# Kernel optimization log

Measured on AMD Instinct MI355X. Metric: run time of the kernel, lower is better.

## Reference

```python
import jax, jax.numpy as jnp
import numpy as np

N_NODES = 100000
N_EDGES = 1600000
IN_CH = 128
HID = 128   # 2 * out_channels
OUT_CH = 64


def setup_inputs() -> dict:
    key = jax.random.key(0)
    k1, k2, k3, k4, k5, k6 = jax.random.split(key, 6)
    x = jax.random.normal(k1, (N_NODES, IN_CH), dtype=jnp.float32)
    edge_index = jax.random.randint(k2, (2, N_EDGES), 0, N_NODES, dtype=jnp.int64)
    W1 = jax.random.normal(k3, (IN_CH, HID), dtype=jnp.float32) / np.sqrt(IN_CH)
    b1 = jax.random.normal(k4, (HID,), dtype=jnp.float32) * 0.01
    W2 = jax.random.normal(k5, (HID, OUT_CH), dtype=jnp.float32) / np.sqrt(HID)
    b2 = jax.random.normal(k6, (OUT_CH,), dtype=jnp.float32) * 0.01
    return {"x": x, "edge_index": edge_index, "W1": W1, "b1": b1, "W2": W2, "b2": b2}


def _gcn_layer(x, src, dst, norm, W, b, n_nodes):
    # GCNConv: linear transform, then normalized scatter-add aggregation + bias
    h = x @ W                                   # [N, d_out]
    msg = h[src] * norm[:, None]                # gather + edge normalize, [E+N, d_out]
    out = jax.ops.segment_sum(msg, dst, num_segments=n_nodes)
    return out + b


def reference(x, edge_index, W1, b1, W2, b2):
    n = x.shape[0]
    loop = jnp.arange(n, dtype=edge_index.dtype)
    # add self-loops (PyG GCNConv default)
    src = jnp.concatenate([edge_index[0], loop])
    dst = jnp.concatenate([edge_index[1], loop])
    # symmetric normalization deg^-1/2[src] * deg^-1/2[dst]
    deg = jax.ops.segment_sum(jnp.ones_like(dst, x.dtype), dst, num_segments=n)
    dinv = jnp.where(deg > 0, jax.lax.rsqrt(deg), 0.0)
    norm = dinv[src] * dinv[dst]

    h = jax.nn.relu(_gcn_layer(x, src, dst, norm, W1, b1, n))
    out = jax.nn.relu(_gcn_layer(h, src, dst, norm, W2, b2, n))
    return out
```

## Files before the change

### kernel.cpp

```cpp
#include <hip/hip_runtime.h>
#include <hip/hip_fp16.h>

typedef _Float16 f16x8 __attribute__((ext_vector_type(8)));
typedef _Float16 f16x4 __attribute__((ext_vector_type(4)));
typedef float f32x4 __attribute__((ext_vector_type(4)));

#define BSH 9
#define BSZ 512
#define CAP 12288

__global__ __launch_bounds__(256) void passA(const int* __restrict__ ei,
                                             int* __restrict__ bcount, int E, int NB) {
  __shared__ int hist[256];
  int t = threadIdx.x;
  hist[t] = 0;
  __syncthreads();
  for (int e = blockIdx.x * 256 + t; e < E; e += gridDim.x * 256)
    atomicAdd(&hist[ei[E + e] >> BSH], 1);
  __syncthreads();
  if (t < NB && hist[t]) atomicAdd(&bcount[t], hist[t]);
}

__global__ __launch_bounds__(256) void scanB(const int* __restrict__ bcount,
                                             int* __restrict__ bstart,
                                             int* __restrict__ bfill, int NB, int E) {
  __shared__ int s[256];
  int t = threadIdx.x;
  int v = (t < NB) ? bcount[t] : 0;
  s[t] = v;
  __syncthreads();
  for (int off = 1; off < 256; off <<= 1) {
    int add = (t >= off) ? s[t - off] : 0;
    __syncthreads();
    s[t] += add;
    __syncthreads();
  }
  if (t < NB) {
    int ex = s[t] - v;
    bstart[t] = ex;
    bfill[t] = ex;
  }
  if (t == 0) bstart[NB] = E;
}

template <int NC, int NWC, bool IN_F16, bool SCALE>
__device__ __forceinline__ void gemm_mfma_body(
    const void* __restrict__ Xv, const float* __restrict__ W,
    const float* __restrict__ dinv, _Float16* __restrict__ G, int nrows, int bid,
    _Float16* Bs) {
  int t = threadIdx.x;
  {
    int n = t % NC;
    int kh = (t / NC) * (NC / 2);
    constexpr int NBLK = (NC / 2) / 8;
#pragma unroll
    for (int b = 0; b < NBLK; ++b) {
      f16x8 tmp;
#pragma unroll
      for (int j = 0; j < 8; ++j)
        tmp[j] = (_Float16)W[(size_t)(kh + b * 8 + j) * NC + n];
      *(f16x8*)(&Bs[n * 136 + kh + b * 8]) = tmp;
    }
  }
  __syncthreads();

  int w = t >> 6, lane = t & 63;
  int m = lane & 15, q = lane >> 4;
  int wr = (w / NWC) * 64, wc = (w % NWC) * 64;
  int row0 = bid * ((4 / NWC) * 64);

  f32x4 acc[4][4];
#pragma unroll
  for (int rt = 0; rt < 4; ++rt)
#pragma unroll
    for (int ct = 0; ct < 4; ++ct)
#pragma unroll
      for (int qq = 0; qq < 4; ++qq) acc[rt][ct][qq] = 0.f;

#pragma unroll
  for (int kc = 0; kc < 4; ++kc) {
    int kbase = kc * 32 + q * 8;
    f16x8 af[4];
#pragma unroll
    for (int rt = 0; rt < 4; ++rt) {
      int row = row0 + wr + rt * 16 + m;
      if constexpr (IN_F16) {
        f16x8 a = {0, 0, 0, 0, 0, 0, 0, 0};
        if (row < nrows) a = *(const f16x8*)((const _Float16*)Xv + (size_t)row * 128 + kbase);
        af[rt] = a;
      } else {
        float4 x0 = {0, 0, 0, 0}, x1 = {0, 0, 0, 0};
        if (row < nrows) {
          const float* Xf = (const float*)Xv;
          x0 = *(const float4*)(Xf + (size_t)row * 128 + kbase);
          x1 = *(const float4*)(Xf + (size_t)row * 128 + kbase + 4);
        }
        f16x8 a;
        a[0] = (_Float16)x0.x; a[1] = (_Float16)x0.y;
        a[2] = (_Float16)x0.z; a[3] = (_Float16)x0.w;
        a[4] = (_Float16)x1.x; a[5] = (_Float16)x1.y;
        a[6] = (_Float16)x1.z; a[7] = (_Float16)x1.w;
        af[rt] = a;
      }
    }
    f16x8 bf[4];
#pragma unroll
    for (int ct = 0; ct < 4; ++ct) {
      int n = wc + ct * 16 + m;
      bf[ct] = *(f16x8*)(&Bs[n * 136 + kbase]);
    }
#pragma unroll
    for (int rt = 0; rt < 4; ++rt)
#pragma unroll
      for (int ct = 0; ct < 4; ++ct)
        acc[rt][ct] = __builtin_amdgcn_mfma_f32_16x16x32_f16(af[rt], bf[ct],
                                                             acc[rt][ct], 0, 0, 0);
  }
#pragma unroll
  for (int rt = 0; rt < 4; ++rt) {
#pragma unroll
    for (int r = 0; r < 4; ++r) {
      int row = row0 + wr + rt * 16 + q * 4 + r;
      if (row < nrows) {
        float d = SCALE ? dinv[row] : 1.f;
#pragma unroll
        for (int ct = 0; ct < 4; ++ct) {
          int col = wc + ct * 16 + m;
          G[(size_t)row * NC + col] = (_Float16)(acc[rt][ct][r] * d);
        }
      }
    }
  }
}

__global__ __launch_bounds__(256) void fused_gemm_passB(
    const float* __restrict__ X, const float* __restrict__ W1,
    _Float16* __restrict__ G, int nrows, int GB,
    const int* __restrict__ ei, int* __restrict__ bfill,
    unsigned int* __restrict__ pairs, int E, int PB) {
  __shared__ char smem[128 * 136 * 2];
  int g = blockIdx.x;
  int M2 = 2 * (GB < PB ? GB : PB);
  bool is_gemm;
  int bid;
  if (g < M2) { is_gemm = (g & 1) == 0; bid = g >> 1; }
  else        { is_gemm = (GB > PB);    bid = g - M2 + (GB < PB ? GB : PB); }
  if (is_gemm) {
    gemm_mfma_body<128, 2, false, false>(X, W1, nullptr, G, nrows, bid,
                                         (_Float16*)smem);
  } else {
    int* hist = (int*)smem;
    int* gbase = (int*)(smem + 1024);
    int t = threadIdx.x;
    hist[t] = 0;
    __syncthreads();
    int d[8], s[8], lp[8], bb[8];
    int base = bid * 2048;
#pragma unroll
    for (int u = 0; u < 8; ++u) {
      int e = base + u * 256 + t;
      if (e < E) {
        d[u] = ei[E + e];
        s[u] = ei[e];
        bb[u] = d[u] >> BSH;
        lp[u] = atomicAdd(&hist[bb[u]], 1);
      } else {
        bb[u] = -1;
      }
    }
    __syncthreads();
    if (hist[t]) gbase[t] = atomicAdd(&bfill[t], hist[t]);
    __syncthreads();
#pragma unroll
    for (int u = 0; u < 8; ++u)
      if (bb[u] >= 0)
        pairs[gbase[bb[u]] + lp[u]] =
            ((unsigned int)(d[u] & (BSZ - 1)) << 17) | (unsigned int)s[u];
  }
}

__global__ __launch_bounds__(256) void gemm2_mfma(const _Float16* __restrict__ X,
                                                  const float* __restrict__ W,
                                                  const float* __restrict__ dinv,
                                                  _Float16* __restrict__ G, int nrows) {
  __shared__ _Float16 Bs[64 * 136];
  gemm_mfma_body<64, 1, true, true>(X, W, dinv, G, nrows, blockIdx.x, Bs);
}

__global__ __launch_bounds__(512) void passC(const unsigned int* __restrict__ pairs,
                                             const int* __restrict__ bstart,
                                             int* __restrict__ rowstart,
                                             int* __restrict__ deg,
                                             float* __restrict__ dinv,
                                             int* __restrict__ csr, int N) {
  __shared__ int hcnt[BSZ];
  __shared__ int lfill[BSZ];
  __shared__ int ss[512];
  __shared__ int lcsr[CAP];
  int b = blockIdx.x;
  int t = threadIdx.x;
  int lo = bstart[b], hi = bstart[b + 1];
  int cnt = hi - lo;
  int nbase = b << BSH;
  hcnt[t] = 0;
  __syncthreads();
  for (int k = lo + t; k < hi; k += 512)
    atomicAdd(&hcnt[(pairs[k] >> 17) & (BSZ - 1)], 1);
  __syncthreads();
  int v = hcnt[t];
  ss[t] = v;
  __syncthreads();
  for (int off = 1; off < 512; off <<= 1) {
    int add = (t >= off) ? ss[t - off] : 0;
    __syncthreads();
    ss[t] += add;
    __syncthreads();
  }
  int ex = ss[t] - v;
  lfill[t] = ex;
  int node = nbase + t;
  if (node < N) {
    rowstart[node] = lo + ex;
    deg[node] = v;
    dinv[node] = rsqrtf((float)(v + 1));
  }
  __syncthreads();
  bool fits = (cnt <= CAP);
  for (int k = lo + t; k < hi; k += 512) {
    unsigned int p = pairs[k];
    int pos = atomicAdd(&lfill[(p >> 17) & (BSZ - 1)], 1);
    int src = (int)(p & 0x1FFFFu);
    if (fits) lcsr[pos] = src;
    else      csr[lo + pos] = src;
  }
  __syncthreads();
  if (fits)
    for (int k = t; k < cnt; k += 512) csr[lo + k] = lcsr[k];
}

__global__ __launch_bounds__(256) void agg128(
    const __half* __restrict__ G, const int* __restrict__ csr,
    const int* __restrict__ rowstart, const int* __restrict__ deg,
    const float* __restrict__ dinv, const float* __restrict__ bias,
    __half* __restrict__ out, int n) {
  int wid = blockIdx.x * 4 + (threadIdx.x >> 6);
  if (wid >= n) return;
  int i = __builtin_amdgcn_readfirstlane(wid);
  int lane = threadIdx.x & 63;
  int g = lane >> 4;
  int c = lane & 15;
  const _Float16* Gh = (const _Float16*)G;
  float di = dinv[i];
  f16x8 self = *(const f16x8*)(Gh + (size_t)i * 128 + c * 8);
  float wself = (g == 0) ? di : 0.f;
  float a[8];
#pragma unroll
  for (int j = 0; j < 8; ++j) a[j] = wself * (float)self[j];
  int s = rowstart[i];
  int d = deg[i];
  for (int base = 0; base < d; base += 64) {
    int chunk = d - base;
    if (chunk > 64) chunk = 64;
    int myidx = (lane < chunk) ? csr[s + base + lane] : i;
    for (int k = 0; k < chunk; k += 8) {
      int sl0 = k + g, sl1 = k + 4 + g;
      int s0 = __shfl(myidx, sl0);
      int s1 = __shfl(myidx, sl1);
      float w0 = dinv[s0];
      float w1 = dinv[s1];
      if (sl0 >= chunk) w0 = 0.f;
      if (sl1 >= chunk) w1 = 0.f;
      f16x8 v0 = *(const f16x8*)(Gh + (size_t)s0 * 128 + c * 8);
      f16x8 v1 = *(const f16x8*)(Gh + (size_t)s1 * 128 + c * 8);
#pragma unroll
      for (int j = 0; j < 8; ++j) a[j] = fmaf(w0, (float)v0[j], a[j]);
#pragma unroll
      for (int j = 0; j < 8; ++j) a[j] = fmaf(w1, (float)v1[j], a[j]);
    }
  }
#pragma unroll
  for (int j = 0; j < 8; ++j) {
    a[j] += __shfl_xor(a[j], 16);
    a[j] += __shfl_xor(a[j], 32);
  }
  if (g == 0) {
    float4 b0 = *(const float4*)(bias + c * 8);
    float4 b1 = *(const float4*)(bias + c * 8 + 4);
    f16x8 r;
    r[0] = (_Float16)fmaxf(fmaf(di, a[0], b0.x), 0.f);
    r[1] = (_Float16)fmaxf(fmaf(di, a[1], b0.y), 0.f);
    r[2] = (_Float16)fmaxf(fmaf(di, a[2], b0.z), 0.f);
    r[3] = (_Float16)fmaxf(fmaf(di, a[3], b0.w), 0.f);
    r[4] = (_Float16)fmaxf(fmaf(di, a[4], b1.x), 0.f);
    r[5] = (_Float16)fmaxf(fmaf(di, a[5], b1.y), 0.f);
    r[6] = (_Float16)fmaxf(fmaf(di, a[6], b1.z), 0.f);
    r[7] = (_Float16)fmaxf(fmaf(di, a[7], b1.w), 0.f);
    *(f16x8*)((_Float16*)out + (size_t)i * 128 + c * 8) = r;
  }
}

__global__ __launch_bounds__(256) void agg64(
    const __half* __restrict__ G, const int* __restrict__ csr,
    const int* __restrict__ rowstart, const int* __restrict__ deg,
    const float* __restrict__ dinv, const float* __restrict__ bias,
    float* __restrict__ out, int n) {
  int wid = blockIdx.x * 4 + (threadIdx.x >> 6);
  if (wid >= n) return;
  int i = __builtin_amdgcn_readfirstlane(wid);
  int lane = threadIdx.x & 63;
  int g = lane >> 4;
  int c = lane & 15;
  const _Float16* Gh = (const _Float16*)G;
  f16x4 self = *(const f16x4*)(Gh + (size_t)i * 64 + c * 4);
  float wself = (g == 0) ? 1.f : 0.f;
  float a[4];
#pragma unroll
  for (int j = 0; j < 4; ++j) a[j] = wself * (float)self[j];
  int s = rowstart[i];
  int d = deg[i];
  for (int base = 0; base < d; base += 64) {
    int chunk = d - base;
    if (chunk > 64) chunk = 64;
    int myidx = (lane < chunk) ? csr[s + base + lane] : i;
    for (int k = 0; k < chunk; k += 8) {
      int sl0 = k + g, sl1 = k + 4 + g;
      int s0 = __shfl(myidx, sl0);
      int s1 = __shfl(myidx, sl1);
      float w0 = (sl0 < chunk) ? 1.f : 0.f;
      float w1 = (sl1 < chunk) ? 1.f : 0.f;
      f16x4 v0 = *(const f16x4*)(Gh + (size_t)s0 * 64 + c * 4);
      f16x4 v1 = *(const f16x4*)(Gh + (size_t)s1 * 64 + c * 4);
#pragma unroll
      for (int j = 0; j < 4; ++j) a[j] = fmaf(w0, (float)v0[j], a[j]);
#pragma unroll
      for (int j = 0; j < 4; ++j) a[j] = fmaf(w1, (float)v1[j], a[j]);
    }
  }
#pragma unroll
  for (int j = 0; j < 4; ++j) {
    a[j] += __shfl_xor(a[j], 16);
    a[j] += __shfl_xor(a[j], 32);
  }
  if (g == 0) {
    float di = dinv[i];
    float4 bv = *(const float4*)(bias + c * 4);
    float4 r;
    r.x = fmaxf(fmaf(di, a[0], bv.x), 0.f);
    r.y = fmaxf(fmaf(di, a[1], bv.y), 0.f);
    r.z = fmaxf(fmaf(di, a[2], bv.z), 0.f);
    r.w = fmaxf(fmaf(di, a[3], bv.w), 0.f);
    *(float4*)(out + (size_t)i * 64 + c * 4) = r;
  }
}

extern "C" void kernel_launch(void* const* d_in, const int* in_sizes, int n_in,
                              void* d_out, int out_size, void* d_ws, size_t ws_size,
                              hipStream_t stream) {
  const float* x  = (const float*)d_in[0];
  const int*   ei = (const int*)d_in[1];
  const float* W1 = (const float*)d_in[2];
  const float* b1 = (const float*)d_in[3];
  const float* W2 = (const float*)d_in[4];
  const float* b2 = (const float*)d_in[5];
  float* out = (float*)d_out;

  const int N = in_sizes[0] / 128;
  const int E = in_sizes[1] / 2;
  const int NB = (N + BSZ - 1) >> BSH;

  char* base = (char*)d_ws;
  size_t off = 0;
  auto alloc = [&](size_t bytes) -> void* {
    void* p = base + off;
    off += (bytes + 255) & ~(size_t)255;
    return p;
  };
  int*          bcount   = (int*)alloc(256 * 4);
  int*          bstart   = (int*)alloc(260 * 4);
  int*          bfill    = (int*)alloc(256 * 4);
  int*          deg      = (int*)alloc((size_t)N * 4);
  int*          rowstart = (int*)alloc((size_t)N * 4);
  float*        dinv     = (float*)alloc((size_t)N * 4);
  int*          csr      = (int*)alloc((size_t)E * 4);
  unsigned int* pairs    = (unsigned int*)alloc((size_t)E * 4);
  __half*       g1       = (__half*)alloc((size_t)N * 128 * 2);
  __half*       x2       = (__half*)alloc((size_t)N * 128 * 2);

  hipMemsetAsync(bcount, 0, 256 * 4, stream);
  passA<<<512, 256, 0, stream>>>(ei, bcount, E, NB);
  scanB<<<1, 256, 0, stream>>>(bcount, bstart, bfill, NB, E);

  int GB = (N + 127) / 128;
  int PB = (E + 2047) / 2048;
  fused_gemm_passB<<<GB + PB, 256, 0, stream>>>(x, W1, (_Float16*)g1, N, GB, ei,
                                                bfill, pairs, E, PB);
  passC<<<NB, 512, 0, stream>>>(pairs, bstart, rowstart, deg, dinv, csr, N);

  agg128<<<(N + 3) / 4, 256, 0, stream>>>(g1, csr, rowstart, deg, dinv, b1, x2, N);
  int G2B = (N + 255) / 256;
  gemm2_mfma<<<G2B, 256, 0, stream>>>((const _Float16*)x2, W2, dinv,
                                      (_Float16*)g1, N);
  agg64<<<(N + 3) / 4, 256, 0, stream>>>(g1, csr, rowstart, deg, dinv, b2, out, N);
}
```

Measured before the change: 282.4 us.

## Compute degrees early and fold source normalization into layer-1 GEMM

Degree counting moves into passA using global atomics, so the layer-1 GEMM can pre-scale rows by deg^-1/2. This lets agg128 drop its per-neighbor dinv gather and do plain sums. The dinv array is removed, and each kernel recomputes rsqrt from deg. Both aggregation kernels gain a 16-neighbor unrolled inner loop to raise memory-level parallelism. The cost is 1.6M global atomics in passA plus an extra memset.

```diff
diff --git a/kernel.cpp b/kernel.cpp
--- a/kernel.cpp
+++ b/kernel.cpp
@@ -1,5 +1,6 @@
 #include <hip/hip_runtime.h>
 #include <hip/hip_fp16.h>
+#include <math.h>
 
 typedef _Float16 f16x8 __attribute__((ext_vector_type(8)));
 typedef _Float16 f16x4 __attribute__((ext_vector_type(4)));
@@ -10,13 +11,17 @@
 #define CAP 12288
 
 __global__ __launch_bounds__(256) void passA(const int* __restrict__ ei,
-                                             int* __restrict__ bcount, int E, int NB) {
+                                             int* __restrict__ bcount,
+                                             int* __restrict__ deg, int E, int NB) {
   __shared__ int hist[256];
   int t = threadIdx.x;
   hist[t] = 0;
   __syncthreads();
-  for (int e = blockIdx.x * 256 + t; e < E; e += gridDim.x * 256)
-    atomicAdd(&hist[ei[E + e] >> BSH], 1);
+  for (int e = blockIdx.x * 256 + t; e < E; e += gridDim.x * 256) {
+    int d = ei[E + e];
+    atomicAdd(&hist[d >> BSH], 1);
+    atomicAdd(&deg[d], 1);
+  }
   __syncthreads();
   if (t < NB && hist[t]) atomicAdd(&bcount[t], hist[t]);
 }
@@ -46,7 +51,7 @@
 template <int NC, int NWC, bool IN_F16, bool SCALE>
 __device__ __forceinline__ void gemm_mfma_body(
     const void* __restrict__ Xv, const float* __restrict__ W,
-    const float* __restrict__ dinv, _Float16* __restrict__ G, int nrows, int bid,
+    const int* __restrict__ deg, _Float16* __restrict__ G, int nrows, int bid,
     _Float16* Bs) {
   int t = threadIdx.x;
   {
@@ -122,7 +127,7 @@
     for (int r = 0; r < 4; ++r) {
       int row = row0 + wr + rt * 16 + q * 4 + r;
       if (row < nrows) {
-        float d = SCALE ? dinv[row] : 1.f;
+        float d = SCALE ? rsqrtf((float)deg[row] + 1.f) : 1.f;
 #pragma unroll
         for (int ct = 0; ct < 4; ++ct) {
           int col = wc + ct * 16 + m;
@@ -135,7 +140,7 @@
 
 __global__ __launch_bounds__(256) void fused_gemm_passB(
     const float* __restrict__ X, const float* __restrict__ W1,
-    _Float16* __restrict__ G, int nrows, int GB,
+    const int* __restrict__ deg, _Float16* __restrict__ G, int nrows, int GB,
     const int* __restrict__ ei, int* __restrict__ bfill,
     unsigned int* __restrict__ pairs, int E, int PB) {
   __shared__ char smem[128 * 136 * 2];
@@ -146,8 +151,8 @@
   if (g < M2) { is_gemm = (g & 1) == 0; bid = g >> 1; }
   else        { is_gemm = (GB > PB);    bid = g - M2 + (GB < PB ? GB : PB); }
   if (is_gemm) {
-    gemm_mfma_body<128, 2, false, false>(X, W1, nullptr, G, nrows, bid,
-                                         (_Float16*)smem);
+    gemm_mfma_body<128, 2, false, true>(X, W1, deg, G, nrows, bid,
+                                        (_Float16*)smem);
   } else {
     int* hist = (int*)smem;
     int* gbase = (int*)(smem + 1024);
@@ -181,17 +186,15 @@
 
 __global__ __launch_bounds__(256) void gemm2_mfma(const _Float16* __restrict__ X,
                                                   const float* __restrict__ W,
-                                                  const float* __restrict__ dinv,
+                                                  const int* __restrict__ deg,
                                                   _Float16* __restrict__ G, int nrows) {
   __shared__ _Float16 Bs[64 * 136];
-  gemm_mfma_body<64, 1, true, true>(X, W, dinv, G, nrows, blockIdx.x, Bs);
+  gemm_mfma_body<64, 1, true, true>(X, W, deg, G, nrows, blockIdx.x, Bs);
 }
 
 __global__ __launch_bounds__(512) void passC(const unsigned int* __restrict__ pairs,
                                              const int* __restrict__ bstart,
                                              int* __restrict__ rowstart,
-                                             int* __restrict__ deg,
-                                             float* __restrict__ dinv,
                                              int* __restrict__ csr, int N) {
   __shared__ int hcnt[BSZ];
   __shared__ int lfill[BSZ];
@@ -219,11 +222,7 @@
   int ex = ss[t] - v;
   lfill[t] = ex;
   int node = nbase + t;
-  if (node < N) {
-    rowstart[node] = lo + ex;
-    deg[node] = v;
-    dinv[node] = rsqrtf((float)(v + 1));
-  }
+  if (node < N) rowstart[node] = lo + ex;
   __syncthreads();
   bool fits = (cnt <= CAP);
   for (int k = lo + t; k < hi; k += 512) {
@@ -241,8 +240,7 @@
 __global__ __launch_bounds__(256) void agg128(
     const __half* __restrict__ G, const int* __restrict__ csr,
     const int* __restrict__ rowstart, const int* __restrict__ deg,
-    const float* __restrict__ dinv, const float* __restrict__ bias,
-    __half* __restrict__ out, int n) {
+    const float* __restrict__ bias, __half* __restrict__ out, int n) {
   int wid = blockIdx.x * 4 + (threadIdx.x >> 6);
   if (wid >= n) return;
   int i = __builtin_amdgcn_readfirstlane(wid);
@@ -250,26 +248,43 @@
   int g = lane >> 4;
   int c = lane & 15;
   const _Float16* Gh = (const _Float16*)G;
-  float di = dinv[i];
+  int d = deg[i];
+  int s = rowstart[i];
+  float di = rsqrtf((float)d + 1.f);
   f16x8 self = *(const f16x8*)(Gh + (size_t)i * 128 + c * 8);
-  float wself = (g == 0) ? di : 0.f;
+  float wself = (g == 0) ? 1.f : 0.f;
   float a[8];
 #pragma unroll
   for (int j = 0; j < 8; ++j) a[j] = wself * (float)self[j];
-  int s = rowstart[i];
-  int d = deg[i];
   for (int base = 0; base < d; base += 64) {
     int chunk = d - base;
     if (chunk > 64) chunk = 64;
     int myidx = (lane < chunk) ? csr[s + base + lane] : i;
-    for (int k = 0; k < chunk; k += 8) {
+    int k = 0;
+    for (; k + 15 < chunk; k += 16) {
+      int s0 = __shfl(myidx, k + g);
+      int s1 = __shfl(myidx, k + 4 + g);
+      int s2 = __shfl(myidx, k + 8 + g);
+      int s3 = __shfl(myidx, k + 12 + g);
+      f16x8 v0 = *(const f16x8*)(Gh + (size_t)s0 * 128 + c * 8);
+      f16x8 v1 = *(const f16x8*)(Gh + (size_t)s1 * 128 + c * 8);
+      f16x8 v2 = *(const f16x8*)(Gh + (size_t)s2 * 128 + c * 8);
+      f16x8 v3 = *(const f16x8*)(Gh + (size_t)s3 * 128 + c * 8);
+#pragma unroll
+      for (int j = 0; j < 8; ++j) a[j] += (float)v0[j];
+#pragma unroll
+      for (int j = 0; j < 8; ++j) a[j] += (float)v1[j];
+#pragma unroll
+      for (int j = 0; j < 8; ++j) a[j] += (float)v2[j];
+#pragma unroll
+      for (int j = 0; j < 8; ++j) a[j] += (float)v3[j];
+    }
+    for (; k < chunk; k += 8) {
       int sl0 = k + g, sl1 = k + 4 + g;
       int s0 = __shfl(myidx, sl0);
       int s1 = __shfl(myidx, sl1);
-      float w0 = dinv[s0];
-      float w1 = dinv[s1];
-      if (sl0 >= chunk) w0 = 0.f;
-      if (sl1 >= chunk) w1 = 0.f;
+      float w0 = (sl0 < chunk) ? 1.f : 0.f;
+      float w1 = (sl1 < chunk) ? 1.f : 0.f;
       f16x8 v0 = *(const f16x8*)(Gh + (size_t)s0 * 128 + c * 8);
       f16x8 v1 = *(const f16x8*)(Gh + (size_t)s1 * 128 + c * 8);
 #pragma unroll
@@ -302,8 +317,7 @@
 __global__ __launch_bounds__(256) void agg64(
     const __half* __restrict__ G, const int* __restrict__ csr,
     const int* __restrict__ rowstart, const int* __restrict__ deg,
-    const float* __restrict__ dinv, const float* __restrict__ bias,
-    float* __restrict__ out, int n) {
+    const float* __restrict__ bias, float* __restrict__ out, int n) {
   int wid = blockIdx.x * 4 + (threadIdx.x >> 6);
   if (wid >= n) return;
   int i = __builtin_amdgcn_readfirstlane(wid);
@@ -311,18 +325,38 @@
   int g = lane >> 4;
   int c = lane & 15;
   const _Float16* Gh = (const _Float16*)G;
+  int d = deg[i];
+  int s = rowstart[i];
+  float di = rsqrtf((float)d + 1.f);
   f16x4 self = *(const f16x4*)(Gh + (size_t)i * 64 + c * 4);
   float wself = (g == 0) ? 1.f : 0.f;
   float a[4];
 #pragma unroll
   for (int j = 0; j < 4; ++j) a[j] = wself * (float)self[j];
-  int s = rowstart[i];
-  int d = deg[i];
   for (int base = 0; base < d; base += 64) {
     int chunk = d - base;
     if (chunk > 64) chunk = 64;
     int myidx = (lane < chunk) ? csr[s + base + lane] : i;
-    for (int k = 0; k < chunk; k += 8) {
+    int k = 0;
+    for (; k + 15 < chunk; k += 16) {
+      int s0 = __shfl(myidx, k + g);
+      int s1 = __shfl(myidx, k + 4 + g);
+      int s2 = __shfl(myidx, k + 8 + g);
+      int s3 = __shfl(myidx, k + 12 + g);
+      f16x4 v0 = *(const f16x4*)(Gh + (size_t)s0 * 64 + c * 4);
+      f16x4 v1 = *(const f16x4*)(Gh + (size_t)s1 * 64 + c * 4);
+      f16x4 v2 = *(const f16x4*)(Gh + (size_t)s2 * 64 + c * 4);
+      f16x4 v3 = *(const f16x4*)(Gh + (size_t)s3 * 64 + c * 4);
+#pragma unroll
+      for (int j = 0; j < 4; ++j) a[j] += (float)v0[j];
+#pragma unroll
+      for (int j = 0; j < 4; ++j) a[j] += (float)v1[j];
+#pragma unroll
+      for (int j = 0; j < 4; ++j) a[j] += (float)v2[j];
+#pragma unroll
+      for (int j = 0; j < 4; ++j) a[j] += (float)v3[j];
+    }
+    for (; k < chunk; k += 8) {
       int sl0 = k + g, sl1 = k + 4 + g;
       int s0 = __shfl(myidx, sl0);
       int s1 = __shfl(myidx, sl1);
@@ -342,7 +376,6 @@
     a[j] += __shfl_xor(a[j], 32);
   }
   if (g == 0) {
-    float di = dinv[i];
     float4 bv = *(const float4*)(bias + c * 4);
     float4 r;
     r.x = fmaxf(fmaf(di, a[0], bv.x), 0.f);
@@ -380,25 +413,25 @@
   int*          bfill    = (int*)alloc(256 * 4);
   int*          deg      = (int*)alloc((size_t)N * 4);
   int*          rowstart = (int*)alloc((size_t)N * 4);
-  float*        dinv     = (float*)alloc((size_t)N * 4);
   int*          csr      = (int*)alloc((size_t)E * 4);
   unsigned int* pairs    = (unsigned int*)alloc((size_t)E * 4);
   __half*       g1       = (__half*)alloc((size_t)N * 128 * 2);
   __half*       x2       = (__half*)alloc((size_t)N * 128 * 2);
 
   hipMemsetAsync(bcount, 0, 256 * 4, stream);
-  passA<<<512, 256, 0, stream>>>(ei, bcount, E, NB);
+  hipMemsetAsync(deg, 0, (size_t)N * 4, stream);
+  passA<<<512, 256, 0, stream>>>(ei, bcount, deg, E, NB);
   scanB<<<1, 256, 0, stream>>>(bcount, bstart, bfill, NB, E);
 
   int GB = (N + 127) / 128;
   int PB = (E + 2047) / 2048;
-  fused_gemm_passB<<<GB + PB, 256, 0, stream>>>(x, W1, (_Float16*)g1, N, GB, ei,
-                                                bfill, pairs, E, PB);
-  passC<<<NB, 512, 0, stream>>>(pairs, bstart, rowstart, deg, dinv, csr, N);
-
-  agg128<<<(N + 3) / 4, 256, 0, stream>>>(g1, csr, rowstart, deg, dinv, b1, x2, N);
+  fused_gemm_passB<<<GB + PB, 256, 0, stream>>>(x, W1, deg, (_Float16*)g1, N, GB,
+                                                ei, bfill, pairs, E, PB);
+  passC<<<NB, 512, 0, stream>>>(pairs, bstart, rowstart, csr, N);
+
+  agg128<<<(N + 3) / 4, 256, 0, stream>>>(g1, csr, rowstart, deg, b1, x2, N);
   int G2B = (N + 255) / 256;
-  gemm2_mfma<<<G2B, 256, 0, stream>>>((const _Float16*)x2, W2, dinv,
+  gemm2_mfma<<<G2B, 256, 0, stream>>>((const _Float16*)x2, W2, deg,
                                       (_Float16*)g1, N);
-  agg64<<<(N + 3) / 4, 256, 0, stream>>>(g1, csr, rowstart, deg, dinv, b2, out, N);
-}
+  agg64<<<(N + 3) / 4, 256, 0, stream>>>(g1, csr, rowstart, deg, b2, out, N);
+}
```

Result: slower. 358.6 us (+27.0%).

## Halve CSR bucket size, prefetch GEMM A fragments, stage GEMM output through LDS

Applied to the files above, without the earlier changes.

The destination bucket size drops from 512 to 256 nodes, so there are twice as many passC blocks and histograms grow to 512 entries. passC loses its large LDS staging buffer and writes CSR entries straight to global memory. The GEMM body now prefetches the next K-chunk of A fragments while issuing MFMAs, and writes its output tile through LDS so global stores are coalesced 16-byte writes. This trades scattered 2-byte stores and low passC parallelism for extra LDS traffic and synchronisation, and scattered global CSR writes could hurt locality.

```diff
diff --git a/kernel.cpp b/kernel.cpp
--- a/kernel.cpp
+++ b/kernel.cpp
@@ -1,35 +1,37 @@
 #include <hip/hip_runtime.h>
 #include <hip/hip_fp16.h>
+#include <math.h>
 
 typedef _Float16 f16x8 __attribute__((ext_vector_type(8)));
-typedef _Float16 f16x4 __attribute__((ext_vector_type(4)));
 typedef float f32x4 __attribute__((ext_vector_type(4)));
 
-#define BSH 9
-#define BSZ 512
-#define CAP 12288
+#define BSH 8
+#define BSZ 256
 
 __global__ __launch_bounds__(256) void passA(const int* __restrict__ ei,
                                              int* __restrict__ bcount, int E, int NB) {
-  __shared__ int hist[256];
+  __shared__ int hist[512];
   int t = threadIdx.x;
   hist[t] = 0;
+  hist[t + 256] = 0;
   __syncthreads();
   for (int e = blockIdx.x * 256 + t; e < E; e += gridDim.x * 256)
     atomicAdd(&hist[ei[E + e] >> BSH], 1);
   __syncthreads();
   if (t < NB && hist[t]) atomicAdd(&bcount[t], hist[t]);
-}
-
-__global__ __launch_bounds__(256) void scanB(const int* __restrict__ bcount,
+  int t2 = t + 256;
+  if (t2 < NB && hist[t2]) atomicAdd(&bcount[t2], hist[t2]);
+}
+
+__global__ __launch_bounds__(512) void scanB(const int* __restrict__ bcount,
                                              int* __restrict__ bstart,
                                              int* __restrict__ bfill, int NB, int E) {
-  __shared__ int s[256];
+  __shared__ int s[512];
   int t = threadIdx.x;
   int v = (t < NB) ? bcount[t] : 0;
   s[t] = v;
   __syncthreads();
-  for (int off = 1; off < 256; off <<= 1) {
+  for (int off = 1; off < 512; off <<= 1) {
     int add = (t >= off) ? s[t - off] : 0;
     __syncthreads();
     s[t] += add;
@@ -67,27 +69,20 @@
   int w = t >> 6, lane = t & 63;
   int m = lane & 15, q = lane >> 4;
   int wr = (w / NWC) * 64, wc = (w % NWC) * 64;
-  int row0 = bid * ((4 / NWC) * 64);
-
-  f32x4 acc[4][4];
-#pragma unroll
-  for (int rt = 0; rt < 4; ++rt)
-#pragma unroll
-    for (int ct = 0; ct < 4; ++ct)
-#pragma unroll
-      for (int qq = 0; qq < 4; ++qq) acc[rt][ct][qq] = 0.f;
-
-#pragma unroll
-  for (int kc = 0; kc < 4; ++kc) {
+  constexpr int ROWS = (4 / NWC) * 64;
+  int row0 = bid * ROWS;
+
+  auto loadA = [&](int kc, f16x8* dst) {
     int kbase = kc * 32 + q * 8;
-    f16x8 af[4];
 #pragma unroll
     for (int rt = 0; rt < 4; ++rt) {
       int row = row0 + wr + rt * 16 + m;
       if constexpr (IN_F16) {
         f16x8 a = {0, 0, 0, 0, 0, 0, 0, 0};
-        if (row < nrows) a = *(const f16x8*)((const _Float16*)Xv + (size_t)row * 128 + kbase);
-        af[rt] = a;
+        if (row < nrows)
+          a = *(const f16x8*)((const _Float16*)Xv + (size_t)row * NC * (128 / NC) +
+                              kbase);
+        dst[rt] = a;
       } else {
         float4 x0 = {0, 0, 0, 0}, x1 = {0, 0, 0, 0};
         if (row < nrows) {
@@ -100,9 +95,26 @@
         a[2] = (_Float16)x0.z; a[3] = (_Float16)x0.w;
         a[4] = (_Float16)x1.x; a[5] = (_Float16)x1.y;
         a[6] = (_Float16)x1.z; a[7] = (_Float16)x1.w;
-        af[rt] = a;
+        dst[rt] = a;
       }
     }
+  };
+
+  f32x4 acc[4][4];
+#pragma unroll
+  for (int rt = 0; rt < 4; ++rt)
+#pragma unroll
+    for (int ct = 0; ct < 4; ++ct)
+#pragma unroll
+      for (int qq = 0; qq < 4; ++qq) acc[rt][ct][qq] = 0.f;
+
+  f16x8 af[4];
+  loadA(0, af);
+#pragma unroll
+  for (int kc = 0; kc < 4; ++kc) {
+    f16x8 afn[4];
+    if (kc < 3) loadA(kc + 1, afn);
+    int kbase = kc * 32 + q * 8;
     f16x8 bf[4];
 #pragma unroll
     for (int ct = 0; ct < 4; ++ct) {
@@ -115,21 +127,35 @@
       for (int ct = 0; ct < 4; ++ct)
         acc[rt][ct] = __builtin_amdgcn_mfma_f32_16x16x32_f16(af[rt], bf[ct],
                                                              acc[rt][ct], 0, 0, 0);
-  }
+    if (kc < 3) {
+#pragma unroll
+      for (int rt = 0; rt < 4; ++rt) af[rt] = afn[rt];
+    }
+  }
+
+  __syncthreads();
+  _Float16* Ct = Bs;
+  constexpr int CPITCH = NC + 8;
 #pragma unroll
   for (int rt = 0; rt < 4; ++rt) {
 #pragma unroll
     for (int r = 0; r < 4; ++r) {
-      int row = row0 + wr + rt * 16 + q * 4 + r;
-      if (row < nrows) {
-        float d = SCALE ? dinv[row] : 1.f;
-#pragma unroll
-        for (int ct = 0; ct < 4; ++ct) {
-          int col = wc + ct * 16 + m;
-          G[(size_t)row * NC + col] = (_Float16)(acc[rt][ct][r] * d);
-        }
-      }
-    }
+      int lrow = wr + rt * 16 + q * 4 + r;
+      int grow = row0 + lrow;
+      float d = 1.f;
+      if (SCALE) d = (grow < nrows) ? dinv[grow] : 1.f;
+#pragma unroll
+      for (int ct = 0; ct < 4; ++ct)
+        Ct[lrow * CPITCH + wc + ct * 16 + m] = (_Float16)(acc[rt][ct][r] * d);
+    }
+  }
+  __syncthreads();
+  constexpr int C8 = NC / 8;
+  for (int idx = t; idx < ROWS * C8; idx += 256) {
+    int lrow = idx / C8, c8 = (idx % C8) * 8;
+    int grow = row0 + lrow;
+    if (grow < nrows)
+      *(f16x8*)(G + (size_t)grow * NC + c8) = *(const f16x8*)(Ct + lrow * CPITCH + c8);
   }
 }
 
@@ -150,9 +176,10 @@
                                          (_Float16*)smem);
   } else {
     int* hist = (int*)smem;
-    int* gbase = (int*)(smem + 1024);
+    int* gbase = (int*)(smem + 2048);
     int t = threadIdx.x;
     hist[t] = 0;
+    hist[t + 256] = 0;
     __syncthreads();
     int d[8], s[8], lp[8], bb[8];
     int base = bid * 2048;
@@ -170,6 +197,8 @@
     }
     __syncthreads();
     if (hist[t]) gbase[t] = atomicAdd(&bfill[t], hist[t]);
+    int t2 = t + 256;
+    if (hist[t2]) gbase[t2] = atomicAdd(&bfill[t2], hist[t2]);
     __syncthreads();
 #pragma unroll
     for (int u = 0; u < 8; ++u)
@@ -183,8 +212,9 @@
                                                   const float* __restrict__ W,
                                                   const float* __restrict__ dinv,
                                                   _Float16* __restrict__ G, int nrows) {
-  __shared__ _Float16 Bs[64 * 136];
-  gemm_mfma_body<64, 1, true, true>(X, W, dinv, G, nrows, blockIdx.x, Bs);
+  __shared__ char smem2[256 * 72 * 2];
+  gemm_mfma_body<64, 1, true, true>(X, W, dinv, G, nrows, blockIdx.x,
+                                    (_Float16*)smem2);
 }
 
 __global__ __launch_bounds__(512) void passC(const unsigned int* __restrict__ pairs,
@@ -195,47 +225,44 @@
                                              int* __restrict__ csr, int N) {
   __shared__ int hcnt[BSZ];
   __shared__ int lfill[BSZ];
-  __shared__ int ss[512];
-  __shared__ int lcsr[CAP];
+  __shared__ int ss[BSZ];
   int b = blockIdx.x;
   int t = threadIdx.x;
   int lo = bstart[b], hi = bstart[b + 1];
-  int cnt = hi - lo;
   int nbase = b << BSH;
-  hcnt[t] = 0;
+  if (t < BSZ) hcnt[t] = 0;
   __syncthreads();
   for (int k = lo + t; k < hi; k += 512)
     atomicAdd(&hcnt[(pairs[k] >> 17) & (BSZ - 1)], 1);
   __syncthreads();
-  int v = hcnt[t];
-  ss[t] = v;
-  __syncthreads();
-  for (int off = 1; off < 512; off <<= 1) {
-    int add = (t >= off) ? ss[t - off] : 0;
-    __syncthreads();
-    ss[t] += add;
-    __syncthreads();
-  }
-  int ex = ss[t] - v;
-  lfill[t] = ex;
-  int node = nbase + t;
-  if (node < N) {
-    rowstart[node] = lo + ex;
-    deg[node] = v;
-    dinv[node] = rsqrtf((float)(v + 1));
-  }
-  __syncthreads();
-  bool fits = (cnt <= CAP);
+  int v = 0;
+  if (t < BSZ) {
+    v = hcnt[t];
+    ss[t] = v;
+  }
+  __syncthreads();
+  for (int off = 1; off < BSZ; off <<= 1) {
+    int add = (t < BSZ && t >= off) ? ss[t - off] : 0;
+    __syncthreads();
+    if (t < BSZ) ss[t] += add;
+    __syncthreads();
+  }
+  if (t < BSZ) {
+    int ex = ss[t] - v;
+    lfill[t] = ex;
+    int node = nbase + t;
+    if (node < N) {
+      rowstart[node] = lo + ex;
+      deg[node] = v;
+      dinv[node] = rsqrtf((float)v + 1.f);
+    }
+  }
+  __syncthreads();
   for (int k = lo + t; k < hi; k += 512) {
     unsigned int p = pairs[k];
     int pos = atomicAdd(&lfill[(p >> 17) & (BSZ - 1)], 1);
-    int src = (int)(p & 0x1FFFFu);
-    if (fits) lcsr[pos] = src;
-    else      csr[lo + pos] = src;
-  }
-  __syncthreads();
-  if (fits)
-    for (int k = t; k < cnt; k += 512) csr[lo + k] = lcsr[k];
+    csr[lo + pos] = (int)(p & 0x1FFFFu);
+  }
 }
 
 __global__ __launch_bounds__(256) void agg128(
@@ -304,6 +331,7 @@
     const int* __restrict__ rowstart, const int* __restrict__ deg,
     const float* __restrict__ dinv, const float* __restrict__ bias,
     float* __restrict__ out, int n) {
+  typedef _Float16 f16x4 __attribute__((ext_vector_type(4)));
   int wid = blockIdx.x * 4 + (threadIdx.x >> 6);
   if (wid >= n) return;
   int i = __builtin_amdgcn_readfirstlane(wid);
@@ -375,20 +403,20 @@
     off += (bytes + 255) & ~(size_t)255;
     return p;
   };
-  int*          bcount   = (int*)alloc(256 * 4);
-  int*          bstart   = (int*)alloc(260 * 4);
-  int*          bfill    = (int*)alloc(256 * 4);
+  int*          bcount   = (int*)alloc(512 * 4);
+  int*          bstart   = (int*)alloc(516 * 4);
+  int*          bfill    = (int*)alloc(512 * 4);
   int*          deg      = (int*)alloc((size_t)N * 4);
   int*          rowstart = (int*)alloc((size_t)N * 4);
   float*        dinv     = (float*)alloc((size_t)N * 4);
-  int*          csr      = (int*)alloc((size_t)E * 4);
+  int*          csr      = (int*)alloc((size_t)E * 4 + 256);
   unsigned int* pairs    = (unsigned int*)alloc((size_t)E * 4);
   __half*       g1       = (__half*)alloc((size_t)N * 128 * 2);
   __half*       x2       = (__half*)alloc((size_t)N * 128 * 2);
 
-  hipMemsetAsync(bcount, 0, 256 * 4, stream);
+  hipMemsetAsync(bcount, 0, 512 * 4, stream);
   passA<<<512, 256, 0, stream>>>(ei, bcount, E, NB);
-  scanB<<<1, 256, 0, stream>>>(bcount, bstart, bfill, NB, E);
+  scanB<<<1, 512, 0, stream>>>(bcount, bstart, bfill, NB, E);
 
   int GB = (N + 127) / 128;
   int PB = (E + 2047) / 2048;
```

Result: slower. 291.6 us (+3.3%).
